# Performance work log

Measured on AMD Instinct MI355X. Metric: run time of the kernel, lower is better.

## Reference

```python
import jax, jax.numpy as jnp
import numpy as np

EXTENT = 0.5       # init kwarg 'extent'
RES = 256          # init kwarg 'resolution'
BATCH = 8
N_PTS = 65536      # one 256x256 Fourier slice per image


def setup_inputs() -> dict:
    key = jax.random.key(0)
    k1, k2 = jax.random.split(key)
    # coordinates in [-extent, extent]
    x = (jax.random.uniform(k1, (BATCH, N_PTS, 3), dtype=jnp.float32) * 2.0 - 1.0) * EXTENT
    # learned volume parameter, matches 1e-5 * randn init
    volume = 1e-5 * jax.random.normal(k2, (RES, RES, RES), dtype=jnp.float32)
    return {"x": x, "volume": volume}


def _grid_sample_3d(vol, coords):
    """Trilinear grid sample, align_corners=False, padding_mode='zeros'.
    vol: [D, H, W]; coords: [..., 3] with (x, y, z) in [-1, 1] indexing (W, H, D).
    Matches torch.nn.functional.grid_sample(mode='bilinear') for 5D input.
    """
    D, H, W = vol.shape
    gx, gy, gz = coords[..., 0], coords[..., 1], coords[..., 2]
    # unnormalize (align_corners=False): ix = ((x + 1) * W - 1) / 2
    ix = ((gx + 1.0) * W - 1.0) * 0.5
    iy = ((gy + 1.0) * H - 1.0) * 0.5
    iz = ((gz + 1.0) * D - 1.0) * 0.5
    x0 = jnp.floor(ix)
    y0 = jnp.floor(iy)
    z0 = jnp.floor(iz)
    tx = ix - x0  # fractional weights
    ty = iy - y0
    tz = iz - z0
    x0i = x0.astype(jnp.int32)
    y0i = y0.astype(jnp.int32)
    z0i = z0.astype(jnp.int32)

    def corner(dz, dy, dx):
        xi = x0i + dx
        yi = y0i + dy
        zi = z0i + dz
        valid = (xi >= 0) & (xi < W) & (yi >= 0) & (yi < H) & (zi >= 0) & (zi < D)
        v = vol[jnp.clip(zi, 0, D - 1), jnp.clip(yi, 0, H - 1), jnp.clip(xi, 0, W - 1)]
        return jnp.where(valid, v, jnp.zeros((), vol.dtype))

    wx0, wy0, wz0 = 1.0 - tx, 1.0 - ty, 1.0 - tz
    out = (corner(0, 0, 0) * wz0 * wy0 * wx0
           + corner(0, 0, 1) * wz0 * wy0 * tx
           + corner(0, 1, 0) * wz0 * ty * wx0
           + corner(0, 1, 1) * wz0 * ty * tx
           + corner(1, 0, 0) * tz * wy0 * wx0
           + corner(1, 0, 1) * tz * wy0 * tx
           + corner(1, 1, 0) * tz * ty * wx0
           + corner(1, 1, 1) * tz * ty * tx)
    return out


def reference(x, volume):
    # original: grid_sample(100 * volume.repeat(B,...), x/(2*extent)*2)
    #    the linear interpolation (mathematically identical).
    coords = x / EXTENT  # [B, n_pts, 3] in [-1, 1]
    return 100.0 * _grid_sample_3d(volume, coords)  # [B, n_pts]
```

## Files before the change

### kernel.cpp

```cpp
#include <hip/hip_runtime.h>
#include <stdint.h>


#define NSLAB 16
#define OVCAP 16384

typedef float v4f __attribute__((ext_vector_type(4)));

__global__ __launch_bounds__(1024) void scatter_kernel(
    const float* __restrict__ x,
    uint32_t* __restrict__ cur,
    uint32_t* __restrict__ ovn,
    uint32_t* __restrict__ ovbkt,
    v4f* __restrict__ ovrec,
    v4f* __restrict__ recs,
    uint32_t* __restrict__ inv,
    int cap, int n)
{
  __shared__ uint32_t lh[NSLAB];
  __shared__ uint32_t gb[NSLAB];
  int t = threadIdx.x;
  if (t < NSLAB) lh[t] = 0;
  __syncthreads();

  int i = blockIdx.x * 1024 + t;
  bool act = (i < n);
  float ix = 0.f, iy = 0.f, iz = 0.f;
  int b = 0;
  uint32_t lr = 0;
  if (act) {
    float gx = x[3 * i + 0] * 2.0f;
    float gy = x[3 * i + 1] * 2.0f;
    float gz = x[3 * i + 2] * 2.0f;
    ix = ((gx + 1.0f) * 256.0f - 1.0f) * 0.5f;
    iy = ((gy + 1.0f) * 256.0f - 1.0f) * 0.5f;
    iz = ((gz + 1.0f) * 256.0f - 1.0f) * 0.5f;
    int z0 = (int)floorf(iz);
    b = min(max(z0, 0), 255) >> 4;
    lr = atomicAdd(&lh[b], 1u);
  }
  __syncthreads();

  if (t < NSLAB) {
    uint32_t c = lh[t];
    gb[t] = c ? atomicAdd(&cur[t], c) : 0u;
  }
  __syncthreads();

  if (act) {
    uint32_t p = gb[b] + lr;
    if (p < (uint32_t)cap) {
      uint32_t slot = (uint32_t)b * cap + p;
      v4f r = { ix, iy, iz, 0.0f };
      recs[slot] = r;
      inv[i] = slot;
    } else {
      uint32_t o = atomicAdd(ovn, 1u);
      if (o < OVCAP) {
        ovbkt[o] = (uint32_t)b;
        v4f r = { ix, iy, iz, __uint_as_float((uint32_t)i) };
        ovrec[o] = r;
      }
      inv[i] = 0xFFFFFFFFu;
    }
  }
}

__device__ __forceinline__ float trilerp_g(
    const float* __restrict__ vol, float ix, float iy, float iz)
{
  float x0f = floorf(ix), y0f = floorf(iy), z0f = floorf(iz);
  float tx = ix - x0f, ty = iy - y0f, tz = iz - z0f;
  int x0 = (int)x0f, y0 = (int)y0f, z0 = (int)z0f;
  float wx0 = (x0 >= 0 && x0 < 256) ? (1.0f - tx) : 0.0f;
  float wx1 = (x0 + 1 >= 0 && x0 + 1 < 256) ? tx : 0.0f;
  float wy0 = (y0 >= 0 && y0 < 256) ? (1.0f - ty) : 0.0f;
  float wy1 = (y0 + 1 >= 0 && y0 + 1 < 256) ? ty : 0.0f;
  float wz0 = (z0 >= 0 && z0 < 256) ? (1.0f - tz) : 0.0f;
  float wz1 = (z0 + 1 >= 0 && z0 + 1 < 256) ? tz : 0.0f;
  int xc0 = min(max(x0, 0), 255), xc1 = min(max(x0 + 1, 0), 255);
  int yc0 = min(max(y0, 0), 255), yc1 = min(max(y0 + 1, 0), 255);
  int zc0 = min(max(z0, 0), 255), zc1 = min(max(z0 + 1, 0), 255);
  int r00 = (zc0 * 256 + yc0) * 256;
  int r01 = (zc0 * 256 + yc1) * 256;
  int r10 = (zc1 * 256 + yc0) * 256;
  int r11 = (zc1 * 256 + yc1) * 256;
  float v000 = vol[r00 + xc0], v001 = vol[r00 + xc1];
  float v010 = vol[r01 + xc0], v011 = vol[r01 + xc1];
  float v100 = vol[r10 + xc0], v101 = vol[r10 + xc1];
  float v110 = vol[r11 + xc0], v111 = vol[r11 + xc1];
  float c00 = v000 * wx0 + v001 * wx1;
  float c01 = v010 * wx0 + v011 * wx1;
  float c10 = v100 * wx0 + v101 * wx1;
  float c11 = v110 * wx0 + v111 * wx1;
  float c0 = c00 * wy0 + c01 * wy1;
  float c1 = c10 * wy0 + c11 * wy1;
  return 100.0f * (c0 * wz0 + c1 * wz1);
}

#define BLK_PER_SLAB 64

__global__ __launch_bounds__(512) void gather_kernel(
    const float* __restrict__ vol,
    const v4f* __restrict__ recs,
    const uint32_t* __restrict__ cur,
    const uint32_t* __restrict__ ovn,
    const uint32_t* __restrict__ ovbkt,
    const v4f* __restrict__ ovrec,
    float* __restrict__ result,
    float* __restrict__ out,
    float* __restrict__ sink,
    int cap)
{
  int phase = blockIdx.x >> 9;
  int w = blockIdx.x & 511;
  int s = phase * 8 + (w & 7);
  int jb = w >> 3;

  const v4f* slab4 = (const v4f*)(vol + (size_t)s * 16 * 256 * 256);
  float acc = 0.0f;
  int base = jb * 4096;
  for (int e = threadIdx.x; e < 4096; e += 512) {
    v4f v = slab4[base + e];
    acc += v.x + v.y + v.z + v.w;
  }
  if (__float_as_uint(acc) == 0xDEADBEEFu) *sink = acc;

  uint32_t cnt = min(cur[s], (uint32_t)cap);
  const v4f* rb = recs + (size_t)s * cap;
  float* resb = result + (size_t)s * cap;
  for (uint32_t j = jb * 512 + threadIdx.x; j < cnt; j += BLK_PER_SLAB * 512) {
    v4f r = __builtin_nontemporal_load(&rb[j]);
    resb[j] = trilerp_g(vol, r.x, r.y, r.z);
  }

  uint32_t nov = min(*ovn, (uint32_t)OVCAP);
  if (jb == 0) {
    for (uint32_t j = threadIdx.x; j < nov; j += 512) {
      if (ovbkt[j] == (uint32_t)s) {
        v4f r = ovrec[j];
        out[__float_as_uint(r.w)] = trilerp_g(vol, r.x, r.y, r.z);
      }
    }
  }
}

__global__ __launch_bounds__(256) void combine_kernel(
    const float* __restrict__ result,
    const uint32_t* __restrict__ inv,
    float* __restrict__ out, int n)
{
  int i = blockIdx.x * 256 + threadIdx.x;
  if (i < n) {
    uint32_t s = inv[i];
    if (s != 0xFFFFFFFFu)
      out[i] = result[s];
  }
}

__global__ __launch_bounds__(256) void direct_kernel(
    const float* __restrict__ x, const float* __restrict__ vol,
    float* __restrict__ out, int n)
{
  int i = blockIdx.x * blockDim.x + threadIdx.x;
  if (i >= n) return;
  float gx = x[3 * i + 0] * 2.0f;
  float gy = x[3 * i + 1] * 2.0f;
  float gz = x[3 * i + 2] * 2.0f;
  float ix = ((gx + 1.0f) * 256.0f - 1.0f) * 0.5f;
  float iy = ((gy + 1.0f) * 256.0f - 1.0f) * 0.5f;
  float iz = ((gz + 1.0f) * 256.0f - 1.0f) * 0.5f;
  out[i] = trilerp_g(vol, ix, iy, iz);
}

extern "C" void kernel_launch(void* const* d_in, const int* in_sizes, int n_in,
                              void* d_out, int out_size, void* d_ws, size_t ws_size,
                              hipStream_t stream) {
  const float* x   = (const float*)d_in[0];
  const float* vol = (const float*)d_in[1];
  float* out = (float*)d_out;
  int n = out_size;

  int m = (n + NSLAB - 1) / NSLAB;
  int cap = m + m / 4 + 64;

  const size_t ovbkt_off = 8192;
  const size_t ovrec_off = ovbkt_off + OVCAP * 4;
  size_t recs_off  = ovrec_off + (size_t)OVCAP * 16;
  size_t recs_b    = (size_t)NSLAB * cap * 16;
  size_t res_off   = recs_off + recs_b;
  size_t res_b     = (size_t)NSLAB * cap * 4;
  size_t inv_off   = res_off + res_b;
  size_t need      = inv_off + (size_t)n * 4;

  if (ws_size >= need && n == 524288) {
    char* ws = (char*)d_ws;
    uint32_t* cur   = (uint32_t*)(ws + 0);
    uint32_t* ovn   = (uint32_t*)(ws + 4096);
    float*    sink  = (float*)(ws + 6144);
    uint32_t* ovbkt = (uint32_t*)(ws + ovbkt_off);
    v4f*      ovrec = (v4f*)(ws + ovrec_off);
    v4f*      recs  = (v4f*)(ws + recs_off);
    float*    result= (float*)(ws + res_off);
    uint32_t* inv   = (uint32_t*)(ws + inv_off);

    (void)hipMemsetAsync(ws, 0, 8192, stream);
    scatter_kernel<<<n / 1024, 1024, 0, stream>>>(
        x, cur, ovn, ovbkt, ovrec, recs, inv, cap, n);
    gather_kernel<<<NSLAB * BLK_PER_SLAB, 512, 0, stream>>>(
        vol, recs, cur, ovn, ovbkt, ovrec, result, out, sink, cap);
    combine_kernel<<<(n + 255) / 256, 256, 0, stream>>>(result, inv, out, n);
  } else {
    direct_kernel<<<(n + 255) / 256, 256, 0, stream>>>(x, vol, out, n);
  }
}
```

Baseline: 126.4 us.

## Pin gather slabs to XCCs via hardware ID and work-steal chunks per slab

The gather kernel now reads the hardware XCC id so each chip die prefetches its own z-slab of the volume into its local L2. Records are then pulled in 256-wide chunks from per-slab atomic cursors, and work-stealing lets blocks help finish the other slabs. The single launch is split into two launches, one per group of eight slabs, and results are written with nontemporal stores. This is meant to improve L2 locality on the multi-die MI355X and to balance load. The cost is extra atomics, two barriers per chunk, and an extra kernel launch. It also depends on how blocks get spread across XCCs: the rank is masked to 127, so prefetch coverage assumes about 128 blocks per XCC.

```diff
diff --git a/kernel.cpp b/kernel.cpp
--- a/kernel.cpp
+++ b/kernel.cpp
@@ -6,6 +6,12 @@
 #define OVCAP 16384
 
 typedef float v4f __attribute__((ext_vector_type(4)));
+
+__device__ __forceinline__ int xcc_id() {
+  unsigned v;
+  asm volatile("s_getreg_b32 %0, hwreg(HW_REG_XCC_ID)" : "=s"(v));
+  return (int)(v & 7);
+}
 
 __global__ __launch_bounds__(1024) void scatter_kernel(
     const float* __restrict__ x,
@@ -98,49 +104,62 @@
   return 100.0f * (c0 * wz0 + c1 * wz1);
 }
 
-#define BLK_PER_SLAB 64
-
-__global__ __launch_bounds__(512) void gather_kernel(
+__global__ __launch_bounds__(256) void gather_kernel(
     const float* __restrict__ vol,
     const v4f* __restrict__ recs,
     const uint32_t* __restrict__ cur,
+    uint32_t* __restrict__ rank,
+    uint32_t* __restrict__ cursor,
     const uint32_t* __restrict__ ovn,
     const uint32_t* __restrict__ ovbkt,
     const v4f* __restrict__ ovrec,
     float* __restrict__ result,
     float* __restrict__ out,
     float* __restrict__ sink,
-    int cap)
-{
-  int phase = blockIdx.x >> 9;
-  int w = blockIdx.x & 511;
-  int s = phase * 8 + (w & 7);
-  int jb = w >> 3;
-
-  const v4f* slab4 = (const v4f*)(vol + (size_t)s * 16 * 256 * 256);
+    int cap, int phase)
+{
+  __shared__ uint32_t sh_rank, sh_chunk;
+  int xcc = xcc_id();
+  int s_own = phase * 8 + xcc;
+
+  if (threadIdx.x == 0) sh_rank = atomicAdd(&rank[s_own], 1u);
+  __syncthreads();
+  uint32_t r = sh_rank & 127;
+
+  const v4f* slab4 = (const v4f*)(vol + (size_t)s_own * 16 * 65536);
   float acc = 0.0f;
-  int base = jb * 4096;
-  for (int e = threadIdx.x; e < 4096; e += 512) {
-    v4f v = slab4[base + e];
+  for (int e = 0; e < 8; ++e) {
+    v4f v = slab4[r * 2048 + e * 256 + threadIdx.x];
     acc += v.x + v.y + v.z + v.w;
   }
   if (__float_as_uint(acc) == 0xDEADBEEFu) *sink = acc;
 
-  uint32_t cnt = min(cur[s], (uint32_t)cap);
-  const v4f* rb = recs + (size_t)s * cap;
-  float* resb = result + (size_t)s * cap;
-  for (uint32_t j = jb * 512 + threadIdx.x; j < cnt; j += BLK_PER_SLAB * 512) {
-    v4f r = __builtin_nontemporal_load(&rb[j]);
-    resb[j] = trilerp_g(vol, r.x, r.y, r.z);
+  for (int t = 0; t < 8; ++t) {
+    int s = phase * 8 + ((xcc + t) & 7);
+    uint32_t cnt = min(cur[s], (uint32_t)cap);
+    const v4f* rb = recs + (size_t)s * cap;
+    float* resb = result + (size_t)s * cap;
+    while (true) {
+      if (threadIdx.x == 0) sh_chunk = atomicAdd(&cursor[s], 256u);
+      __syncthreads();
+      uint32_t c0 = sh_chunk;
+      __syncthreads();
+      if (c0 >= cnt) break;
+      uint32_t j = c0 + threadIdx.x;
+      if (j < cnt) {
+        v4f rec = __builtin_nontemporal_load(&rb[j]);
+        float v = trilerp_g(vol, rec.x, rec.y, rec.z);
+        __builtin_nontemporal_store(v, &resb[j]);
+      }
+    }
   }
 
   uint32_t nov = min(*ovn, (uint32_t)OVCAP);
-  if (jb == 0) {
-    for (uint32_t j = threadIdx.x; j < nov; j += 512) {
-      if (ovbkt[j] == (uint32_t)s) {
-        v4f r = ovrec[j];
-        out[__float_as_uint(r.w)] = trilerp_g(vol, r.x, r.y, r.z);
-      }
+  for (uint32_t j = threadIdx.x; j < nov; j += 256) {
+    uint32_t b = ovbkt[j];
+    if ((int)(b >> 3) == phase) {
+      v4f rr = ovrec[j];
+      out[__float_as_uint(rr.w)] = trilerp_g(vol, rr.x, rr.y, rr.z);
     }
   }
 }
@@ -195,20 +214,24 @@
 
   if (ws_size >= need && n == 524288) {
     char* ws = (char*)d_ws;
-    uint32_t* cur   = (uint32_t*)(ws + 0);
-    uint32_t* ovn   = (uint32_t*)(ws + 4096);
-    float*    sink  = (float*)(ws + 6144);
-    uint32_t* ovbkt = (uint32_t*)(ws + ovbkt_off);
-    v4f*      ovrec = (v4f*)(ws + ovrec_off);
-    v4f*      recs  = (v4f*)(ws + recs_off);
-    float*    result= (float*)(ws + res_off);
-    uint32_t* inv   = (uint32_t*)(ws + inv_off);
+    uint32_t* cur    = (uint32_t*)(ws + 0);
+    uint32_t* rank   = (uint32_t*)(ws + 256);
+    uint32_t* cursor = (uint32_t*)(ws + 512);
+    uint32_t* ovn    = (uint32_t*)(ws + 1024);
+    float*    sink   = (float*)(ws + 6144);
+    uint32_t* ovbkt  = (uint32_t*)(ws + ovbkt_off);
+    v4f*      ovrec  = (v4f*)(ws + ovrec_off);
+    v4f*      recs   = (v4f*)(ws + recs_off);
+    float*    result = (float*)(ws + res_off);
+    uint32_t* inv    = (uint32_t*)(ws + inv_off);
 
     (void)hipMemsetAsync(ws, 0, 8192, stream);
     scatter_kernel<<<n / 1024, 1024, 0, stream>>>(
         x, cur, ovn, ovbkt, ovrec, recs, inv, cap, n);
-    gather_kernel<<<NSLAB * BLK_PER_SLAB, 512, 0, stream>>>(
-        vol, recs, cur, ovn, ovbkt, ovrec, result, out, sink, cap);
+    gather_kernel<<<1024, 256, 0, stream>>>(
+        vol, recs, cur, rank, cursor, ovn, ovbkt, ovrec, result, out, sink, cap, 0);
+    gather_kernel<<<1024, 256, 0, stream>>>(
+        vol, recs, cur, rank, cursor, ovn, ovbkt, ovrec, result, out, sink, cap, 1);
     combine_kernel<<<(n + 255) / 256, 256, 0, stream>>>(result, inv, out, n);
   } else {
     direct_kernel<<<(n + 255) / 256, 256, 0, stream>>>(x, vol, out, n);
```

Measured after the change: 337.2 us. +166.8%, slower.
